# Performance work log

Measured on AMD Instinct MI355X. Metric: run time of the kernel, lower is better.

## Reference

```python
import jax, jax.numpy as jnp
import numpy as np

B, S, D = 8, 2048, 512  # batch, seq_len, d_model (= units*heads = 64*8)


def setup_inputs() -> dict:
    key = jax.random.key(0)
    k1, k2, k3, k4 = jax.random.split(key, 4)
    scale = 1.0 / np.sqrt(D)
    return {
        "data": jax.random.normal(k1, (B, S, D), dtype=jnp.float32),
        "Wq": jax.random.normal(k2, (D, D), dtype=jnp.float32) * scale,
        "Wk": jax.random.normal(k3, (D, D), dtype=jnp.float32) * scale,
        "Wv": jax.random.normal(k4, (D, D), dtype=jnp.float32) * scale,
    }


def reference(data, Wq, Wk, Wv):
    # Bias-free projections (no head split in the original module).
    q = data @ Wq  # [B,S,D]
    k = data @ Wk
    v = data @ Wv
    scores = jnp.einsum("bsd,btd->bst", q, k)  # [B,S,S]
    # NOTE: original scales by sqrt(weight.shape[-1]) == sqrt(seq_len), not sqrt(d_k).
    scores = scores / jnp.sqrt(jnp.float32(scores.shape[-1]))
    # Causal mask: (w + 1e6) * tril - 1e6  ==  where(tril, w, -1e6)
    causal = jnp.tril(jnp.ones((scores.shape[1], scores.shape[2]), dtype=bool))
    scores = jnp.where(causal[None, :, :], scores, jnp.float32(-1e6))
    attn = jax.nn.softmax(scores, axis=-1)
    return jnp.einsum("bst,btd->bsd", attn, v)  # [B,S,D]
```

## Files before the change

kernel.cpp:

```cpp
#include <hip/hip_runtime.h>

typedef unsigned short u16;
typedef __attribute__((ext_vector_type(8))) short short8;
typedef __attribute__((ext_vector_type(4))) float f32x4;


__device__ __forceinline__ u16 f2bf(float f) {
    unsigned u = __float_as_uint(f);
    u += 0x7fffu + ((u >> 16) & 1u);
    return (u16)(u >> 16);
}

__device__ __forceinline__ void lds_cp16(const u16* g, u16* l) {
#if defined(__has_builtin) && __has_builtin(__builtin_amdgcn_global_load_lds)
    __builtin_amdgcn_global_load_lds(
        (const __attribute__((address_space(1))) void*)g,
        (__attribute__((address_space(3))) void*)l, 16, 0, 0);
#else
    *(uint4*)l = *(const uint4*)g;
#endif
}

template <bool ROWSUM>
__device__ __forceinline__ void gemm_core(const u16* __restrict__ Ag, int lda,
                                          const u16* __restrict__ Bg, int ldb,
                                          int ksteps, u16* Alds, u16* Blds,
                                          f32x4 (&acc)[4][4], f32x4* accL) {
    const int t = threadIdx.x;
    const int lane = t & 63;
    const int w = t >> 6;
    const int wr = (w >> 1) * 64;
    const int wc = (w & 1) * 64;
    const int el0 = t * 8;
    const short ob = (short)0x3f80;
    const short8 ones = {ob, ob, ob, ob, ob, ob, ob, ob};

    auto stage = [&](int kt, int buf) {
#pragma unroll
        for (int p = 0; p < 2; ++p) {
            const int el = el0 + p * 2048;
            const int row = el >> 5, col = el & 31;
            lds_cp16(Ag + (size_t)row * lda + kt * 32 + col, Alds + buf * 4096 + el);
            lds_cp16(Bg + (size_t)row * ldb + kt * 32 + col, Blds + buf * 4096 + el);
        }
    };

    stage(0, 0);
    int cur = 0;
    for (int kt = 0; kt < ksteps; ++kt) {
        __syncthreads();
        if (kt + 1 < ksteps) stage(kt + 1, cur ^ 1);
        const short8* A8 = (const short8*)(Alds + cur * 4096);
        const short8* B8 = (const short8*)(Blds + cur * 4096);
        short8 a[4], b[4];
#pragma unroll
        for (int i = 0; i < 4; ++i)
            a[i] = A8[(wr + i * 16 + (lane & 15)) * 4 + (lane >> 4)];
#pragma unroll
        for (int j = 0; j < 4; ++j)
            b[j] = B8[(wc + j * 16 + (lane & 15)) * 4 + (lane >> 4)];
#pragma unroll
        for (int i = 0; i < 4; ++i)
#pragma unroll
            for (int j = 0; j < 4; ++j)
                acc[i][j] = __builtin_amdgcn_mfma_f32_16x16x32_bf16(a[i], b[j], acc[i][j], 0, 0, 0);
        if constexpr (ROWSUM) {
#pragma unroll
            for (int i = 0; i < 4; ++i)
                accL[i] = __builtin_amdgcn_mfma_f32_16x16x32_bf16(a[i], ones, accL[i], 0, 0, 0);
        }
        cur ^= 1;
    }
}


__global__ void k_cvt_x(const float4* __restrict__ X, ushort4* __restrict__ Xb, int n4) {
    for (int i = blockIdx.x * blockDim.x + threadIdx.x; i < n4; i += gridDim.x * blockDim.x) {
        float4 v = X[i];
        ushort4 o;
        o.x = f2bf(v.x); o.y = f2bf(v.y); o.z = f2bf(v.z); o.w = f2bf(v.w);
        Xb[i] = o;
    }
}

__global__ void k_cvt_w(const float* __restrict__ Wq, const float* __restrict__ Wk,
                        const float* __restrict__ Wv, u16* __restrict__ Wt) {
    int idx = blockIdx.x * 256 + threadIdx.x;
    int z = idx >> 18;
    int nk = idx & 262143;
    int n = nk >> 9, k = nk & 511;
    const float* W = (z == 0) ? Wq : (z == 1 ? Wk : Wv);
    float v = W[k * 512 + n];
    if (z == 0) v *= 0.022097086912079608f;
    Wt[idx] = f2bf(v);
}

__global__ __launch_bounds__(256, 4) void k_proj(const u16* __restrict__ Xb, const u16* __restrict__ Wt,
                                                 u16* __restrict__ Qb, u16* __restrict__ Kb,
                                                 u16* __restrict__ Vt) {
    __shared__ alignas(16) u16 Alds[2][4096];
    __shared__ alignas(16) u16 Blds[2][4096];
    const int bid = blockIdx.x;
    const int u = bid >> 3;
    const int z = u >> 6;
    const int nt = (u >> 4) & 3;
    const int mt = (bid & 7) * 16 + (u & 15);
    const u16* Ag = Xb + (size_t)mt * 128 * 512;
    const u16* Bg = Wt + (size_t)z * 512 * 512 + (size_t)nt * 128 * 512;
    f32x4 acc[4][4] = {};
    gemm_core<false>(Ag, 512, Bg, 512, 16, &Alds[0][0], &Blds[0][0], acc, (f32x4*)nullptr);

    const int t = threadIdx.x, lane = t & 63, w = t >> 6;
    const int wr = (w >> 1) * 64, wc = (w & 1) * 64;
    if (z < 2) {
        u16* O = (z == 0) ? Qb : Kb;
#pragma unroll
        for (int i = 0; i < 4; ++i)
#pragma unroll
            for (int j = 0; j < 4; ++j)
#pragma unroll
                for (int r = 0; r < 4; ++r) {
                    int m = mt * 128 + wr + i * 16 + 4 * (lane >> 4) + r;
                    int n = nt * 128 + wc + j * 16 + (lane & 15);
                    O[(size_t)m * 512 + n] = f2bf(acc[i][j][r]);
                }
    } else {
        int b = mt >> 4;
#pragma unroll
        for (int i = 0; i < 4; ++i)
#pragma unroll
            for (int j = 0; j < 4; ++j) {
                int s0 = (mt * 128 + wr + i * 16 + 4 * (lane >> 4)) & 2047;
                int d = nt * 128 + wc + j * 16 + (lane & 15);
                ushort4 pk;
                pk.x = f2bf(acc[i][j][0]); pk.y = f2bf(acc[i][j][1]);
                pk.z = f2bf(acc[i][j][2]); pk.w = f2bf(acc[i][j][3]);
                *(ushort4*)(Vt + (size_t)b * 512 * 2048 + (size_t)d * 2048 + s0) = pk;
            }
    }
}

__global__ __launch_bounds__(256, 4) void k_scores(const u16* __restrict__ Qb, const u16* __restrict__ Kb,
                                                   u16* __restrict__ P) {
    const int bid = blockIdx.x;
    const int bz = bid & 7;
    const int tt = bid >> 3;
    int qi = (int)((sqrtf(8.0f * tt + 1.0f) - 1.0f) * 0.5f);
    while ((qi + 1) * (qi + 2) / 2 <= tt) ++qi;
    while (qi * (qi + 1) / 2 > tt) --qi;
    const int kvj = tt - qi * (qi + 1) / 2;

    __shared__ alignas(16) u16 Alds[2][4096];
    __shared__ alignas(16) u16 Blds[2][4096];
    const u16* Ag = Qb + (size_t)bz * 2048 * 512 + (size_t)qi * 128 * 512;
    const u16* Bg = Kb + (size_t)bz * 2048 * 512 + (size_t)kvj * 128 * 512;
    f32x4 acc[4][4] = {};
    gemm_core<false>(Ag, 512, Bg, 512, 16, &Alds[0][0], &Blds[0][0], acc, (f32x4*)nullptr);

    const int t = threadIdx.x, lane = t & 63, w = t >> 6;
    const int wr = (w >> 1) * 64, wc = (w & 1) * 64;
    u16* Pb = P + (size_t)bz * 2048 * 2048;
#pragma unroll
    for (int i = 0; i < 4; ++i)
#pragma unroll
        for (int j = 0; j < 4; ++j)
#pragma unroll
            for (int r = 0; r < 4; ++r) {
                int q = qi * 128 + wr + i * 16 + 4 * (lane >> 4) + r;
                int kv = kvj * 128 + wc + j * 16 + (lane & 15);
                float pv = (kv <= q) ? __expf(acc[i][j][r]) : 0.0f;
                Pb[(size_t)q * 2048 + kv] = f2bf(pv);
            }
}

__global__ __launch_bounds__(256, 4) void k_pv(const u16* __restrict__ P, const u16* __restrict__ Vt,
                                               float* __restrict__ Out) {
    __shared__ alignas(16) u16 Alds[2][2048];
    __shared__ alignas(16) u16 Blds[2][4096];
    const int bid = blockIdx.x;
    const int bz = bid & 7;
    const int u = bid >> 3;
    const int g = u >> 5;
    const int s = u & 31;
    const int nt = g;
    const int qi2 = (g & 1) ? (31 - s) : s;
    const int ksteps = (qi2 + 1) * 2;

    const int t = threadIdx.x, lane = t & 63, w = t >> 6;
    const int l = lane & 15, g4 = lane >> 4;
    const int wr = (w >> 1) * 32, wc = (w & 1) * 64;
    const u16* Ag = P + (size_t)bz * 2048 * 2048 + (size_t)qi2 * 64 * 2048;
    const u16* Bg = Vt + (size_t)bz * 512 * 2048 + (size_t)nt * 128 * 2048;
    const short ob = (short)0x3f80;
    const short8 ones = {ob, ob, ob, ob, ob, ob, ob, ob};

    auto stage = [&](int kt, int buf) {
        {
            const int el = t * 8;
            const int row = el >> 5, col = el & 31;
            lds_cp16(Ag + (size_t)row * 2048 + kt * 32 + col, &Alds[buf][el]);
        }
#pragma unroll
        for (int p = 0; p < 2; ++p) {
            const int el = t * 8 + p * 2048;
            const int row = el >> 5, col = el & 31;
            lds_cp16(Bg + (size_t)row * 2048 + kt * 32 + col, &Blds[buf][el]);
        }
    };

    f32x4 acc[2][4] = {};
    f32x4 accL[2] = {};
    stage(0, 0);
    int cur = 0;
    for (int kt = 0; kt < ksteps; ++kt) {
        __syncthreads();
        if (kt + 1 < ksteps) stage(kt + 1, cur ^ 1);
        const short8* A8 = (const short8*)&Alds[cur][0];
        const short8* B8 = (const short8*)&Blds[cur][0];
        short8 a[2], b[4];
#pragma unroll
        for (int i = 0; i < 2; ++i) a[i] = A8[(wr + i * 16 + l) * 4 + g4];
#pragma unroll
        for (int j = 0; j < 4; ++j) b[j] = B8[(wc + j * 16 + l) * 4 + g4];
#pragma unroll
        for (int i = 0; i < 2; ++i) {
#pragma unroll
            for (int j = 0; j < 4; ++j)
                acc[i][j] = __builtin_amdgcn_mfma_f32_16x16x32_bf16(a[i], b[j], acc[i][j], 0, 0, 0);
            accL[i] = __builtin_amdgcn_mfma_f32_16x16x32_bf16(a[i], ones, accL[i], 0, 0, 0);
        }
        cur ^= 1;
    }

#pragma unroll
    for (int i = 0; i < 2; ++i) {
        float inv[4];
#pragma unroll
        for (int r = 0; r < 4; ++r) inv[r] = 1.0f / accL[i][r];
#pragma unroll
        for (int j = 0; j < 4; ++j) {
            const int d = nt * 128 + wc + j * 16 + l;
#pragma unroll
            for (int r = 0; r < 4; ++r) {
                const int q = qi2 * 64 + wr + i * 16 + 4 * g4 + r;
                Out[(size_t)bz * 2048 * 512 + (size_t)q * 512 + d] = acc[i][j][r] * inv[r];
            }
        }
    }
}


extern "C" void kernel_launch(void* const* d_in, const int* in_sizes, int n_in,
                              void* d_out, int out_size, void* d_ws, size_t ws_size,
                              hipStream_t stream) {
    const float* data = (const float*)d_in[0];
    const float* Wq = (const float*)d_in[1];
    const float* Wk = (const float*)d_in[2];
    const float* Wv = (const float*)d_in[3];
    float* out = (float*)d_out;
    char* ws = (char*)d_ws;

    u16* Xb = (u16*)(ws);
    u16* Qb = (u16*)(ws + 16777216);
    u16* Kb = (u16*)(ws + 33554432);
    u16* Vt = (u16*)(ws + 50331648);
    u16* Wt = (u16*)(ws + 67108864);
    u16* P  = (u16*)(ws + 68681728);

    k_cvt_x<<<2048, 256, 0, stream>>>((const float4*)data, (ushort4*)Xb, (8 * 2048 * 512) / 4);
    k_cvt_w<<<3072, 256, 0, stream>>>(Wq, Wk, Wv, Wt);
    k_proj<<<1536, 256, 0, stream>>>(Xb, Wt, Qb, Kb, Vt);
    k_scores<<<1088, 256, 0, stream>>>(Qb, Kb, P);
    k_pv<<<1024, 256, 0, stream>>>(P, Vt, out);
}
```

Baseline: 131.7 us.

## Fold Wq·Wkᵀ into one matrix and rework GEMM core with swizzled K=64 tiles

The scores are rewritten as X·(Wq Wkᵀ)·Xᵀ. A small extra GEMM builds the combined 512x512 matrix M (scaled), the projection then computes only G = X·M and V, and the scores kernel multiplies G against the bf16 input X directly. This removes one of the three projection GEMMs and the K write and read. Separately, the shared GEMM core now stages K=64 tiles with an XOR swizzle to avoid LDS bank conflicts. It drops the double-buffered prefetch for a load-then-sync single buffer, which may expose load latency. Rounding M to bf16 adds a little extra numerical error.

Measured after the change: 112.4 us. 1.17x faster.

```diff
diff --git a/kernel.cpp b/kernel.cpp
--- a/kernel.cpp
+++ b/kernel.cpp
@@ -21,55 +21,61 @@
 #endif
 }
 
-template <bool ROWSUM>
-__device__ __forceinline__ void gemm_core(const u16* __restrict__ Ag, int lda,
-                                          const u16* __restrict__ Bg, int ldb,
-                                          int ksteps, u16* Alds, u16* Blds,
-                                          f32x4 (&acc)[4][4], f32x4* accL) {
+template <int MI, bool ROWSUM>
+__device__ __forceinline__ void gemm64(const u16* __restrict__ Ag, int lda,
+                                       const u16* __restrict__ Bg, int ldb,
+                                       int ksteps, u16* Alds, u16* Blds,
+                                       f32x4 (&acc)[MI][4], f32x4* accL) {
     const int t = threadIdx.x;
-    const int lane = t & 63;
-    const int w = t >> 6;
-    const int wr = (w >> 1) * 64;
+    const int lane = t & 63, w = t >> 6;
+    const int l15 = lane & 15, g4 = lane >> 4;
+    const int wr = (w >> 1) * (MI * 16);
     const int wc = (w & 1) * 64;
-    const int el0 = t * 8;
+    const int swz = l15 & 7;
     const short ob = (short)0x3f80;
     const short8 ones = {ob, ob, ob, ob, ob, ob, ob, ob};
 
-    auto stage = [&](int kt, int buf) {
-#pragma unroll
-        for (int p = 0; p < 2; ++p) {
-            const int el = el0 + p * 2048;
-            const int row = el >> 5, col = el & 31;
-            lds_cp16(Ag + (size_t)row * lda + kt * 32 + col, Alds + buf * 4096 + el);
-            lds_cp16(Bg + (size_t)row * ldb + kt * 32 + col, Blds + buf * 4096 + el);
-        }
-    };
-
-    stage(0, 0);
-    int cur = 0;
     for (int kt = 0; kt < ksteps; ++kt) {
         __syncthreads();
-        if (kt + 1 < ksteps) stage(kt + 1, cur ^ 1);
-        const short8* A8 = (const short8*)(Alds + cur * 4096);
-        const short8* B8 = (const short8*)(Blds + cur * 4096);
-        short8 a[4], b[4];
-#pragma unroll
-        for (int i = 0; i < 4; ++i)
-            a[i] = A8[(wr + i * 16 + (lane & 15)) * 4 + (lane >> 4)];
-#pragma unroll
-        for (int j = 0; j < 4; ++j)
-            b[j] = B8[(wc + j * 16 + (lane & 15)) * 4 + (lane >> 4)];
-#pragma unroll
-        for (int i = 0; i < 4; ++i)
-#pragma unroll
-            for (int j = 0; j < 4; ++j)
-                acc[i][j] = __builtin_amdgcn_mfma_f32_16x16x32_bf16(a[i], b[j], acc[i][j], 0, 0, 0);
-        if constexpr (ROWSUM) {
-#pragma unroll
-            for (int i = 0; i < 4; ++i)
-                accL[i] = __builtin_amdgcn_mfma_f32_16x16x32_bf16(a[i], ones, accL[i], 0, 0, 0);
-        }
-        cur ^= 1;
+#pragma unroll
+        for (int p = 0; p < MI; ++p) {
+            const int gi = t + p * 256;
+            const int row = gi >> 3;
+            const int gl = (gi & 7) ^ (row & 7);
+            lds_cp16(Ag + (size_t)row * lda + kt * 64 + gl * 8, Alds + gi * 8);
+        }
+#pragma unroll
+        for (int p = 0; p < 4; ++p) {
+            const int gi = t + p * 256;
+            const int row = gi >> 3;
+            const int gl = (gi & 7) ^ (row & 7);
+            lds_cp16(Bg + (size_t)row * ldb + kt * 64 + gl * 8, Blds + gi * 8);
+        }
+        __syncthreads();
+#pragma unroll
+        for (int ks = 0; ks < 2; ++ks) {
+            short8 a[MI], b[4];
+#pragma unroll
+            for (int i = 0; i < MI; ++i) {
+                const int r = wr + i * 16 + l15;
+                a[i] = *(const short8*)(Alds + r * 64 + (((ks * 4 + g4) ^ swz) * 8));
+            }
+#pragma unroll
+            for (int j = 0; j < 4; ++j) {
+                const int r = wc + j * 16 + l15;
+                b[j] = *(const short8*)(Blds + r * 64 + (((ks * 4 + g4) ^ swz) * 8));
+            }
+#pragma unroll
+            for (int i = 0; i < MI; ++i)
+#pragma unroll
+                for (int j = 0; j < 4; ++j)
+                    acc[i][j] = __builtin_amdgcn_mfma_f32_16x16x32_bf16(a[i], b[j], acc[i][j], 0, 0, 0);
+            if constexpr (ROWSUM) {
+#pragma unroll
+                for (int i = 0; i < MI; ++i)
+                    accL[i] = __builtin_amdgcn_mfma_f32_16x16x32_bf16(a[i], ones, accL[i], 0, 0, 0);
+            }
+        }
     }
 }
 
@@ -87,33 +93,57 @@
                         const float* __restrict__ Wv, u16* __restrict__ Wt) {
     int idx = blockIdx.x * 256 + threadIdx.x;
     int z = idx >> 18;
-    int nk = idx & 262143;
-    int n = nk >> 9, k = nk & 511;
-    const float* W = (z == 0) ? Wq : (z == 1 ? Wk : Wv);
-    float v = W[k * 512 + n];
-    if (z == 0) v *= 0.022097086912079608f;
+    int rem = idx & 262143;
+    float v;
+    if (z == 0) v = Wq[rem];
+    else if (z == 1) v = Wk[rem];
+    else { int n = rem >> 9, k = rem & 511; v = Wv[k * 512 + n]; }
     Wt[idx] = f2bf(v);
 }
 
+__global__ __launch_bounds__(256, 4) void k_gemm_m(const u16* __restrict__ Wt, u16* __restrict__ Mt) {
+    __shared__ alignas(16) u16 Alds[8192];
+    __shared__ alignas(16) u16 Blds[8192];
+    const int mt = blockIdx.x & 3, nt = blockIdx.x >> 2;
+    const u16* Ag = Wt + 0 * 512 * 512 + (size_t)mt * 128 * 512;
+    const u16* Bg = Wt + 1 * 512 * 512 + (size_t)nt * 128 * 512;
+    f32x4 acc[4][4] = {};
+    gemm64<4, false>(Ag, 512, Bg, 512, 8, Alds, Blds, acc, (f32x4*)nullptr);
+
+    const int t = threadIdx.x, lane = t & 63, w = t >> 6;
+    const int wr = (w >> 1) * 64, wc = (w & 1) * 64;
+    const float sc = 0.022097086912079608f;
+#pragma unroll
+    for (int i = 0; i < 4; ++i)
+#pragma unroll
+        for (int j = 0; j < 4; ++j)
+#pragma unroll
+            for (int r = 0; r < 4; ++r) {
+                int e = mt * 128 + wr + i * 16 + 4 * (lane >> 4) + r;
+                int f = nt * 128 + wc + j * 16 + (lane & 15);
+                Mt[(size_t)f * 512 + e] = f2bf(acc[i][j][r] * sc);
+            }
+}
+
 __global__ __launch_bounds__(256, 4) void k_proj(const u16* __restrict__ Xb, const u16* __restrict__ Wt,
-                                                 u16* __restrict__ Qb, u16* __restrict__ Kb,
-                                                 u16* __restrict__ Vt) {
-    __shared__ alignas(16) u16 Alds[2][4096];
-    __shared__ alignas(16) u16 Blds[2][4096];
+                                                 const u16* __restrict__ Mt,
+                                                 u16* __restrict__ Gb, u16* __restrict__ Vt) {
+    __shared__ alignas(16) u16 Alds[8192];
+    __shared__ alignas(16) u16 Blds[8192];
     const int bid = blockIdx.x;
     const int u = bid >> 3;
     const int z = u >> 6;
     const int nt = (u >> 4) & 3;
     const int mt = (bid & 7) * 16 + (u & 15);
     const u16* Ag = Xb + (size_t)mt * 128 * 512;
-    const u16* Bg = Wt + (size_t)z * 512 * 512 + (size_t)nt * 128 * 512;
+    const u16* Bg = (z == 0) ? (Mt + (size_t)nt * 128 * 512)
+                             : (Wt + 2 * 512 * 512 + (size_t)nt * 128 * 512);
     f32x4 acc[4][4] = {};
-    gemm_core<false>(Ag, 512, Bg, 512, 16, &Alds[0][0], &Blds[0][0], acc, (f32x4*)nullptr);
+    gemm64<4, false>(Ag, 512, Bg, 512, 8, Alds, Blds, acc, (f32x4*)nullptr);
 
     const int t = threadIdx.x, lane = t & 63, w = t >> 6;
     const int wr = (w >> 1) * 64, wc = (w & 1) * 64;
-    if (z < 2) {
-        u16* O = (z == 0) ? Qb : Kb;
+    if (z == 0) {
 #pragma unroll
         for (int i = 0; i < 4; ++i)
 #pragma unroll
@@ -122,7 +152,7 @@
                 for (int r = 0; r < 4; ++r) {
                     int m = mt * 128 + wr + i * 16 + 4 * (lane >> 4) + r;
                     int n = nt * 128 + wc + j * 16 + (lane & 15);
-                    O[(size_t)m * 512 + n] = f2bf(acc[i][j][r]);
+                    Gb[(size_t)m * 512 + n] = f2bf(acc[i][j][r]);
                 }
     } else {
         int b = mt >> 4;
@@ -140,7 +170,7 @@
     }
 }
 
-__global__ __launch_bounds__(256, 4) void k_scores(const u16* __restrict__ Qb, const u16* __restrict__ Kb,
+__global__ __launch_bounds__(256, 4) void k_scores(const u16* __restrict__ Gb, const u16* __restrict__ Xb,
                                                    u16* __restrict__ P) {
     const int bid = blockIdx.x;
     const int bz = bid & 7;
@@ -150,12 +180,12 @@
     while (qi * (qi + 1) / 2 > tt) --qi;
     const int kvj = tt - qi * (qi + 1) / 2;
 
-    __shared__ alignas(16) u16 Alds[2][4096];
-    __shared__ alignas(16) u16 Blds[2][4096];
-    const u16* Ag = Qb + (size_t)bz * 2048 * 512 + (size_t)qi * 128 * 512;
-    const u16* Bg = Kb + (size_t)bz * 2048 * 512 + (size_t)kvj * 128 * 512;
+    __shared__ alignas(16) u16 Alds[8192];
+    __shared__ alignas(16) u16 Blds[8192];
+    const u16* Ag = Gb + (size_t)bz * 2048 * 512 + (size_t)qi * 128 * 512;
+    const u16* Bg = Xb + (size_t)bz * 2048 * 512 + (size_t)kvj * 128 * 512;
     f32x4 acc[4][4] = {};
-    gemm_core<false>(Ag, 512, Bg, 512, 16, &Alds[0][0], &Blds[0][0], acc, (f32x4*)nullptr);
+    gemm64<4, false>(Ag, 512, Bg, 512, 8, Alds, Blds, acc, (f32x4*)nullptr);
 
     const int t = threadIdx.x, lane = t & 63, w = t >> 6;
     const int wr = (w >> 1) * 64, wc = (w & 1) * 64;
@@ -175,8 +205,8 @@
 
 __global__ __launch_bounds__(256, 4) void k_pv(const u16* __restrict__ P, const u16* __restrict__ Vt,
                                                float* __restrict__ Out) {
-    __shared__ alignas(16) u16 Alds[2][2048];
-    __shared__ alignas(16) u16 Blds[2][4096];
+    __shared__ alignas(16) u16 Alds[4096];
+    __shared__ alignas(16) u16 Blds[8192];
     const int bid = blockIdx.x;
     const int bz = bid & 7;
     const int u = bid >> 3;
@@ -184,54 +214,17 @@
     const int s = u & 31;
     const int nt = g;
     const int qi2 = (g & 1) ? (31 - s) : s;
-    const int ksteps = (qi2 + 1) * 2;
+    const int ksteps = qi2 + 1;
+
+    const u16* Ag = P + (size_t)bz * 2048 * 2048 + (size_t)qi2 * 64 * 2048;
+    const u16* Bg = Vt + (size_t)bz * 512 * 2048 + (size_t)nt * 128 * 2048;
+    f32x4 acc[2][4] = {};
+    f32x4 accL[2] = {};
+    gemm64<2, true>(Ag, 2048, Bg, 2048, ksteps, Alds, Blds, acc, accL);
 
     const int t = threadIdx.x, lane = t & 63, w = t >> 6;
     const int l = lane & 15, g4 = lane >> 4;
     const int wr = (w >> 1) * 32, wc = (w & 1) * 64;
-    const u16* Ag = P + (size_t)bz * 2048 * 2048 + (size_t)qi2 * 64 * 2048;
-    const u16* Bg = Vt + (size_t)bz * 512 * 2048 + (size_t)nt * 128 * 2048;
-    const short ob = (short)0x3f80;
-    const short8 ones = {ob, ob, ob, ob, ob, ob, ob, ob};
-
-    auto stage = [&](int kt, int buf) {
-        {
-            const int el = t * 8;
-            const int row = el >> 5, col = el & 31;
-            lds_cp16(Ag + (size_t)row * 2048 + kt * 32 + col, &Alds[buf][el]);
-        }
-#pragma unroll
-        for (int p = 0; p < 2; ++p) {
-            const int el = t * 8 + p * 2048;
-            const int row = el >> 5, col = el & 31;
-            lds_cp16(Bg + (size_t)row * 2048 + kt * 32 + col, &Blds[buf][el]);
-        }
-    };
-
-    f32x4 acc[2][4] = {};
-    f32x4 accL[2] = {};
-    stage(0, 0);
-    int cur = 0;
-    for (int kt = 0; kt < ksteps; ++kt) {
-        __syncthreads();
-        if (kt + 1 < ksteps) stage(kt + 1, cur ^ 1);
-        const short8* A8 = (const short8*)&Alds[cur][0];
-        const short8* B8 = (const short8*)&Blds[cur][0];
-        short8 a[2], b[4];
-#pragma unroll
-        for (int i = 0; i < 2; ++i) a[i] = A8[(wr + i * 16 + l) * 4 + g4];
-#pragma unroll
-        for (int j = 0; j < 4; ++j) b[j] = B8[(wc + j * 16 + l) * 4 + g4];
-#pragma unroll
-        for (int i = 0; i < 2; ++i) {
-#pragma unroll
-            for (int j = 0; j < 4; ++j)
-                acc[i][j] = __builtin_amdgcn_mfma_f32_16x16x32_bf16(a[i], b[j], acc[i][j], 0, 0, 0);
-            accL[i] = __builtin_amdgcn_mfma_f32_16x16x32_bf16(a[i], ones, accL[i], 0, 0, 0);
-        }
-        cur ^= 1;
-    }
-
 #pragma unroll
     for (int i = 0; i < 2; ++i) {
         float inv[4];
@@ -261,15 +254,16 @@
     char* ws = (char*)d_ws;
 
     u16* Xb = (u16*)(ws);
-    u16* Qb = (u16*)(ws + 16777216);
-    u16* Kb = (u16*)(ws + 33554432);
+    u16* Gb = (u16*)(ws + 16777216);
+    u16* Mt = (u16*)(ws + 33554432);
     u16* Vt = (u16*)(ws + 50331648);
     u16* Wt = (u16*)(ws + 67108864);
     u16* P  = (u16*)(ws + 68681728);
 
     k_cvt_x<<<2048, 256, 0, stream>>>((const float4*)data, (ushort4*)Xb, (8 * 2048 * 512) / 4);
     k_cvt_w<<<3072, 256, 0, stream>>>(Wq, Wk, Wv, Wt);
-    k_proj<<<1536, 256, 0, stream>>>(Xb, Wt, Qb, Kb, Vt);
-    k_scores<<<1088, 256, 0, stream>>>(Qb, Kb, P);
+    k_gemm_m<<<16, 256, 0, stream>>>(Wt, Mt);
+    k_proj<<<1024, 256, 0, stream>>>(Xb, Wt, Mt, Gb, Vt);
+    k_scores<<<1088, 256, 0, stream>>>(Gb, Xb, P);
     k_pv<<<1024, 256, 0, stream>>>(P, Vt, out);
 }
```
